# Optimization experiments

Measured on AMD Instinct MI355X. Metric: run time of the kernel, lower is better.

Reference implementation:

```python
import jax, jax.numpy as jnp
import numpy as np

NEG = -1e30  # log-space 'zero' that stays finite under autodiff
BLANK = 0


def _logsumexp3(a, b, c):
    m = jnp.maximum(jnp.maximum(a, b), c)
    return m + jnp.log(jnp.exp(a - m) + jnp.exp(b - m) + jnp.exp(c - m))


def setup_inputs() -> dict:
    key = jax.random.key(0)
    k1, k2, k3, k4 = jax.random.split(key, 4)
    T, B, C, S = 1024, 128, 96, 200
    logits = jax.random.normal(k1, (T, B, C), dtype=jnp.float32)
    log_probs = jax.nn.log_softmax(logits, axis=-1)  # CTC expects log-probs
    targets = jax.random.randint(k2, (B, S), 1, C, dtype=jnp.int32)  # labels in [1, C-1]
    input_lengths = jax.random.randint(k3, (B,), T // 2, T + 1, dtype=jnp.int32)
    target_lengths = jax.random.randint(k4, (B,), S // 2, S + 1, dtype=jnp.int32)
    return {"log_probs": log_probs, "targets": targets,
            "input_lengths": input_lengths, "target_lengths": target_lengths}


def ctc_loss(log_probs, targets, input_lengths, target_lengths):
    T, B, C = log_probs.shape
    S = targets.shape[1]
    L = 2 * S + 1  # extended target length (blanks interleaved)

    # Extended target sequence: blank, t0, blank, t1, ..., blank  -> [B, L]
    ext = jnp.zeros((B, L), dtype=targets.dtype).at[:, 1::2].set(targets)
    # Skip transition s-2 -> s allowed when ext[s] != blank and ext[s] != ext[s-2]
    ext_m2 = jnp.pad(ext[:, :-2], ((0, 0), (2, 0)), constant_values=BLANK)
    allow_skip = (ext != BLANK) & (ext != ext_m2) & (jnp.arange(L)[None, :] >= 2)

    emit0 = jnp.take_along_axis(log_probs[0], ext, axis=1)  # [B, L]
    alpha0 = jnp.full((B, L), NEG, dtype=log_probs.dtype)
    alpha0 = alpha0.at[:, 0].set(emit0[:, 0]).at[:, 1].set(emit0[:, 1])

    def step(alpha, lp_t):
        a1 = jnp.pad(alpha[:, :-1], ((0, 0), (1, 0)), constant_values=NEG)
        a2 = jnp.pad(alpha[:, :-2], ((0, 0), (2, 0)), constant_values=NEG)
        a2 = jnp.where(allow_skip, a2, NEG)
        emit = jnp.take_along_axis(lp_t, ext, axis=1)  # [B, L]
        new = _logsumexp3(alpha, a1, a2) + emit
        return new, new

    _, alphas_rest = jax.lax.scan(step, alpha0, log_probs[1:])  # [T-1, B, L]
    alphas = jnp.concatenate([alpha0[None], alphas_rest], axis=0)  # [T, B, L]

    # Gather alpha at t = input_length - 1 for each batch element -> [B, L]
    aT = alphas[input_lengths - 1, jnp.arange(B)]
    s_last = 2 * target_lengths  # index of trailing blank
    end_idx = jnp.stack([s_last - 1, s_last], axis=1)  # [B, 2]
    a_end = jnp.take_along_axis(aT, end_idx, axis=1)  # [B, 2]
    m = jnp.max(a_end, axis=1)
    ll = m + jnp.log(jnp.sum(jnp.exp(a_end - m[:, None]), axis=1))
    loss = -ll
    # zero_infinity=True: zero out non-finite (huge) losses
    loss = jnp.where(loss > 1e29, 0.0, loss)
    # reduction='mean': divide by target lengths, then mean over batch
    return jnp.mean(loss / target_lengths.astype(loss.dtype))


def reference(log_probs, targets, input_lengths, target_lengths):
    return ctc_loss(log_probs, targets, input_lengths, target_lengths)
```

## Files before the change

### kernel.cpp

```cpp
#include <hip/hip_runtime.h>
#include <hip/hip_fp16.h>

#define NEGV  (-1e30f)
#define LOG2E 1.44269504088896340736f
#define LN2F  0.69314718055994530942f

constexpr int Tn = 1024;
constexpr int Bn = 128;
constexpr int Cn = 96;
constexpr int Sn = 200;
constexpr int Ln = 2 * Sn + 1;
constexpr int W  = 7;
constexpr int CH = 16;
constexpr int NCH = Tn / CH;

__device__ __forceinline__ float fexp2(float x) {
#if __has_builtin(__builtin_amdgcn_exp2f)
    return __builtin_amdgcn_exp2f(x);
#else
    return exp2f(x);
#endif
}
__device__ __forceinline__ float flog2(float x) {
#if __has_builtin(__builtin_amdgcn_logf)
    return __builtin_amdgcn_logf(x);
#else
    return __log2f(x);
#endif
}
__device__ __forceinline__ float2 cvt2(unsigned u) {
    const __half2 h = *reinterpret_cast<const __half2*>(&u);
    return __half22float2(h);
}

__device__ __forceinline__ float shup1(float x) {
    return __int_as_float(__builtin_amdgcn_update_dpp(
        0, __float_as_int(x), 0x138, 0xf, 0xf, false));
}

__device__ __forceinline__ float wave_max_dpp_to_lane63(float x) {
    #define DPP_MAX(ctrl)                                                   \
        x = fmaxf(x, __int_as_float(__builtin_amdgcn_update_dpp(            \
                __float_as_int(x), __float_as_int(x), (ctrl), 0xf, 0xf, false)))
    DPP_MAX(0x111);
    DPP_MAX(0x112);
    DPP_MAX(0x114);
    DPP_MAX(0x118);
    DPP_MAX(0x142);
    DPP_MAX(0x143);
    #undef DPP_MAX
    return x;
}

__global__ __launch_bounds__(256, 1) void ctc_fused_kernel(
    const float* __restrict__ lp,
    const int*   __restrict__ tg,
    const int*   __restrict__ il,
    const int*   __restrict__ tl,
    float*       __restrict__ out_pb)
{
    const int b    = blockIdx.x;
    const int w    = threadIdx.x >> 6;
    const int lane = threadIdx.x & 63;

    __shared__ __half buf[2][CH][512];
    __shared__ float  endv[2];

    float a0v = 0.f, a1v = 0.f, a2v = 0.f, a3v = 0.f, a4v = 0.f, a5v = 0.f, a6v = 0.f;
    float pm1 = 0.f, pm2 = 0.f;
    float g0 = 0.f, g1 = 0.f, g2 = 0.f, g3 = 0.f, g4 = 0.f, g5 = 0.f, g6 = 0.f;
    float zl = 0.f, g1z = 0.f, g0z = 0.f;
    int   K = 0, k_cap = 0, t = 1;
    int   inlen = 1 << 30, tlen = 1, ee0 = -1, ee1 = -1;

    int   cidx[W] = {0, 0, 0, 0, 0, 0, 0};
    bool  liv[W]  = {false, false, false, false, false, false, false};
    float rE[6][W];
    int   pw = 0;

#define P_LOAD(CHK)                                                          \
    {                                                                        \
        _Pragma("unroll")                                                    \
        for (int k = 0; k < 6; ++k) {                                        \
            const int r_ = pw + 3 * k;                                       \
            const int t_ = (r_ < CH) ? ((CHK) * CH + r_) : (Tn - 1);         \
            const float* src_ = lp + ((size_t)t_ * Bn + b) * Cn;             \
            _Pragma("unroll")                                                \
            for (int j = 0; j < W; ++j) rE[k][j] = src_[cidx[j]];            \
        }                                                                    \
    }

#define P_GATH(CHK)                                                          \
    {                                                                        \
        const int bb_ = (CHK) & 1;                                           \
        _Pragma("unroll")                                                    \
        for (int k = 0; k < 6; ++k) {                                        \
            const int r_ = pw + 3 * k;                                       \
            if (r_ < CH) {                                                   \
                unsigned us_[8];                                             \
                _Pragma("unroll")                                            \
                for (int j = 0; j < W; ++j) {                                \
                    const float pr_ = liv[j] ? fexp2(rE[k][j] * LOG2E) : 0.0f; \
                    us_[j] = __half_as_ushort(__float2half(pr_));            \
                }                                                            \
                us_[7] = 0;                                                  \
                uint4 v_;                                                    \
                v_.x = us_[0] | (us_[1] << 16);                              \
                v_.y = us_[2] | (us_[3] << 16);                              \
                v_.z = us_[4] | (us_[5] << 16);                              \
                v_.w = us_[6] | (us_[7] << 16);                              \
                *reinterpret_cast<uint4*>(&buf[bb_][r_][lane * 8]) = v_;     \
            }                                                                \
        }                                                                    \
    }

    if (w == 0) {
        if (lane == 0) { endv[0] = 0.0f; endv[1] = 0.0f; }
        inlen = il[b];
        tlen  = tl[b];
        ee0 = 2 * tlen - 1;
        ee1 = 2 * tlen;
        auto mk_gate = [&](int j) -> float {
            const int s = lane * W + j;
            if (s < Ln && (s & 1) && s >= 3) {
                const int kk = s >> 1;
                if (tg[b * Sn + kk] != tg[b * Sn + kk - 1]) return 1.0f;
            }
            return 0.0f;
        };
        g0 = mk_gate(0); g1 = mk_gate(1); g2 = mk_gate(2); g3 = mk_gate(3);
        g4 = mk_gate(4); g5 = mk_gate(5); g6 = mk_gate(6);
        zl  = (lane == 0) ? 0.0f : 1.0f;
        g1z = g1 * zl;
        g0z = g0 * zl;
    } else {
        pw = w - 1;
        #pragma unroll
        for (int j = 0; j < W; ++j) {
            const int s = lane * W + j;
            cidx[j] = (s < Ln && (s & 1)) ? tg[b * Sn + (s >> 1)] : 0;
            liv[j]  = (s < Ln);
        }
        P_LOAD(0);
        P_GATH(0);
        P_LOAD(1);
    }
    __syncthreads();

#define CAP(J, AJ) { const int s_ = lane * W + (J);                          \
                     if (s_ == ee0) endv[0] = (AJ);                          \
                     if (s_ == ee1) endv[1] = (AJ); }

#define CSTEP(V)                                                             \
  {                                                                          \
    float2 f_;                                                               \
    f_ = cvt2((V).x); const float e0m = f_.x, e1m = f_.y;                    \
    f_ = cvt2((V).y); const float e2m = f_.x, e3m = f_.y;                    \
    f_ = cvt2((V).z); const float e4m = f_.x, e5m = f_.y;                    \
    f_ = cvt2((V).w); const float e6m = f_.x;                                \
    const float n6 = fmaf(g6, a4v, a6v + a5v) * e6m;                         \
    const float n5 = fmaf(g5, a3v, a5v + a4v) * e5m;                         \
    const float npm1 = shup1(n6);               \
    const float npm2 = shup1(n5);                                            \
    const float n4 = fmaf(g4, a2v, a4v + a3v) * e4m;                         \
    const float n3 = fmaf(g3, a1v, a3v + a2v) * e3m;                         \
    const float n2 = fmaf(g2, a0v, a2v + a1v) * e2m;                         \
    const float n1 = fmaf(g1z, pm1, a1v + a0v) * e1m;                        \
    const float n0 = fmaf(g0z, pm2, fmaf(zl, pm1, a0v)) * e0m;               \
    a6v = n6; a5v = n5; a4v = n4; a3v = n3; a2v = n2; a1v = n1; a0v = n0;    \
    pm1 = npm1; pm2 = npm2;                                                  \
    if (t == inlen - 1) {                                                    \
      CAP(0, a0v); CAP(1, a1v); CAP(2, a2v); CAP(3, a3v);                    \
      CAP(4, a4v); CAP(5, a5v); CAP(6, a6v);                                 \
      k_cap = K;                                                             \
    }                                                                        \
    ++t;                                                                     \
  }

#define BMAX(J, AJ) { const int s_ = lane * W + (J);                         \
                      if (s_ >= ell && s_ <= ee1) mx = fmaxf(mx, (AJ)); }

#define RESCALE()                                                            \
  {                                                                          \
    const int ell = (2 * tlen - 1) - 2 * (inlen - t);                        \
    float mx = 0.0f;                                                         \
    BMAX(0, a0v); BMAX(1, a1v); BMAX(2, a2v); BMAX(3, a3v);                  \
    BMAX(4, a4v); BMAX(5, a5v); BMAX(6, a6v);                                \
    const float mxr = wave_max_dpp_to_lane63(mx);                            \
    const int  smx = __builtin_amdgcn_readlane(__float_as_int(mxr), 63);     \
    const int  eb  = (smx >> 23) & 0xff;                                     \
    const bool nz  = (smx > 0) && (eb < 255);                                \
    const float scale = nz ? __int_as_float((254 - eb) << 23) : 1.0f;        \
    K += nz ? (127 - eb) : 0;                                                \
    a0v *= scale; a1v *= scale; a2v *= scale; a3v *= scale;                  \
    a4v *= scale; a5v *= scale; a6v *= scale;                                \
    pm1 *= scale; pm2 *= scale;                                              \
  }

    for (int c = 0; c < NCH; ++c) {
        if (w == 0) {
            const uint4* rp =
                reinterpret_cast<const uint4*>(&buf[c & 1][0][0]) + lane;
            uint4 q[8];
            if (c == 0) {
                a0v = (lane == 0) ? __half2float(buf[0][0][0]) : 0.0f;
                a1v = (lane == 0) ? __half2float(buf[0][0][1]) : 0.0f;
                #pragma unroll
                for (int k = 0; k < 8; ++k) q[k] = rp[(k + 1) * 64];
                #pragma unroll
                for (int i = 1; i < CH; ++i) {
                    const uint4 v = q[(i - 1) & 7];
                    if (i < 8) q[(i - 1) & 7] = rp[(i + 8) * 64];
                    CSTEP(v);
                    if (i == 7 || i == 15) RESCALE();
                }
            } else {
                #pragma unroll
                for (int k = 0; k < 8; ++k) q[k] = rp[k * 64];
                #pragma unroll
                for (int i = 0; i < CH; ++i) {
                    const uint4 v = q[i & 7];
                    if (i < 8) q[i & 7] = rp[(i + 8) * 64];
                    CSTEP(v);
                    if (i == 7 || i == 15) RESCALE();
                }
            }
        } else {
            if (c + 1 < NCH) {
                P_GATH(c + 1);
                if (c + 2 < NCH) P_LOAD(c + 2);
            }
        }
        __syncthreads();
    }

#undef RESCALE
#undef BMAX
#undef CSTEP
#undef CAP
#undef P_GATH
#undef P_LOAD

    if (w == 0 && lane == 0) {
        const float sum = endv[0] + endv[1];
        const float ll2 = flog2(sum) - (float)k_cap;
        float lb = -(ll2 * LN2F);
        if (lb > 1e29f || !(lb == lb)) lb = 0.0f;
        out_pb[b] = lb / (float)tlen;
    }
}

__global__ __launch_bounds__(448) void ctc_fallback_kernel(
    const float* __restrict__ lp, const int* __restrict__ tg,
    const int* __restrict__ il, const int* __restrict__ tl,
    float* __restrict__ out_pb)
{
    const int b   = blockIdx.x;
    const int tid = threadIdx.x;

    __shared__ float alpha[2][Ln];
    __shared__ float lprow[2][Cn];
    __shared__ float endv[2];

    const int inlen = il[b];
    const int tlen  = tl[b];
    const int e0 = 2 * tlen - 1;
    const int e1 = 2 * tlen;

    const bool active = (tid < Ln);
    int  myclass = 0;
    bool allow   = false;
    if (active && (tid & 1)) {
        const int k = tid >> 1;
        myclass = tg[b * Sn + k];
        if (tid >= 3) allow = (myclass != tg[b * Sn + k - 1]);
    }

    const float* lpb = lp + (size_t)b * Cn;
    if (tid < Cn) lprow[0][tid] = lpb[tid];

    float vv[4] = {0.f, 0.f, 0.f, 0.f};
    if (tid < Cn) {
        vv[1] = lpb[(size_t)1 * Bn * Cn + tid];
        vv[2] = lpb[(size_t)2 * Bn * Cn + tid];
        vv[3] = lpb[(size_t)3 * Bn * Cn + tid];
        vv[0] = lpb[(size_t)4 * Bn * Cn + tid];
    }
    __syncthreads();
    if (active) alpha[0][tid] = (tid < 2) ? lprow[0][myclass] : NEGV;

    int cur = 0;
    #pragma unroll 4
    for (int t = 1; t < Tn; ++t) {
        if (tid < Cn) {
            lprow[t & 1][tid] = vv[t & 3];
            if (t + 4 < Tn)
                vv[t & 3] = lpb[(size_t)(t + 4) * Bn * Cn + tid];
        }
        __syncthreads();
        if (active) {
            const float a0 = alpha[cur][tid];
            const float a1 = (tid >= 1) ? alpha[cur][tid - 1] : NEGV;
            const float a2 = allow ? alpha[cur][tid - 2] : NEGV;
            const float m  = fmaxf(a0, fmaxf(a1, a2));
            const float nv = m + __logf(__expf(a0 - m) + __expf(a1 - m) + __expf(a2 - m))
                           + lprow[t & 1][myclass];
            alpha[cur ^ 1][tid] = nv;
            if (t == inlen - 1) {
                if (tid == e0) endv[0] = nv;
                if (tid == e1) endv[1] = nv;
            }
        }
        cur ^= 1;
    }
    __syncthreads();

    if (tid == 0) {
        const float x = endv[0], y = endv[1];
        const float m = fmaxf(x, y);
        const float ll = m + __logf(__expf(x - m) + __expf(y - m));
        float lb = -ll;
        if (lb > 1e29f) lb = 0.f;
        out_pb[b] = lb / (float)tlen;
    }
}

__global__ void reduce_mean_kernel(const float* __restrict__ pb,
                                   float* __restrict__ out)
{
    const int l = threadIdx.x;
    float s = pb[l] + pb[l + 64];
    #pragma unroll
    for (int o = 32; o; o >>= 1) s += __shfl_down(s, o);
    if (l == 0) out[0] = s * (1.0f / (float)Bn);
}

extern "C" void kernel_launch(void* const* d_in, const int* in_sizes, int n_in,
                              void* d_out, int out_size, void* d_ws, size_t ws_size,
                              hipStream_t stream)
{
    const float* lp = (const float*)d_in[0];
    const int*   tg = (const int*)d_in[1];
    const int*   il = (const int*)d_in[2];
    const int*   tl = (const int*)d_in[3];
    float* out = (float*)d_out;

    if (ws_size >= 4096) {
        float* pb = (float*)d_ws;
        ctc_fused_kernel<<<Bn, 256, 0, stream>>>(lp, tg, il, tl, pb);
        reduce_mean_kernel<<<1, 64, 0, stream>>>(pb, out);
    } else {
        float* pb = (float*)d_ws;
        ctc_fallback_kernel<<<Bn, 448, 0, stream>>>(lp, tg, il, tl, pb);
        reduce_mean_kernel<<<1, 64, 0, stream>>>(pb, out);
    }
}
```

Before: 201.6 us.

## Double-buffer producer registers and use a lighter LDS-only barrier

Producer waves now hold two register sets, so the global loads for chunk c+2 are issued before the exp/convert/store of chunk c+1 instead of after it. This hides global load latency across a whole chunk rather than only behind the gather. The chunk loop is unrolled by two so the LDS buffer index and register set are compile-time constants. The __syncthreads is replaced by a custom barrier that waits only on lgkmcnt, letting outstanding global loads stay in flight across the barrier. The cost is extra register pressure in the producer waves.

```diff
diff --git a/kernel.cpp b/kernel.cpp
--- a/kernel.cpp
+++ b/kernel.cpp
@@ -52,6 +52,14 @@
     return x;
 }
 
+#define PCBAR()                                                              \
+    do {                                                                     \
+        __builtin_amdgcn_sched_barrier(0);                                   \
+        asm volatile("s_waitcnt lgkmcnt(0)" ::: "memory");                   \
+        __builtin_amdgcn_s_barrier();                                        \
+        __builtin_amdgcn_sched_barrier(0);                                   \
+    } while (0)
+
 __global__ __launch_bounds__(256, 1) void ctc_fused_kernel(
     const float* __restrict__ lp,
     const int*   __restrict__ tg,
@@ -75,10 +83,10 @@
 
     int   cidx[W] = {0, 0, 0, 0, 0, 0, 0};
     bool  liv[W]  = {false, false, false, false, false, false, false};
-    float rE[6][W];
+    float rEA[6][W], rEB[6][W];
     int   pw = 0;
 
-#define P_LOAD(CHK)                                                          \
+#define P_LOAD_SET(CHK, RS)                                                  \
     {                                                                        \
         _Pragma("unroll")                                                    \
         for (int k = 0; k < 6; ++k) {                                        \
@@ -86,11 +94,11 @@
             const int t_ = (r_ < CH) ? ((CHK) * CH + r_) : (Tn - 1);         \
             const float* src_ = lp + ((size_t)t_ * Bn + b) * Cn;             \
             _Pragma("unroll")                                                \
-            for (int j = 0; j < W; ++j) rE[k][j] = src_[cidx[j]];            \
+            for (int j = 0; j < W; ++j) RS[k][j] = src_[cidx[j]];            \
         }                                                                    \
     }
 
-#define P_GATH(CHK)                                                          \
+#define P_GATH_SET(CHK, RS)                                                  \
     {                                                                        \
         const int bb_ = (CHK) & 1;                                           \
         _Pragma("unroll")                                                    \
@@ -100,7 +108,7 @@
                 unsigned us_[8];                                             \
                 _Pragma("unroll")                                            \
                 for (int j = 0; j < W; ++j) {                                \
-                    const float pr_ = liv[j] ? fexp2(rE[k][j] * LOG2E) : 0.0f; \
+                    const float pr_ = liv[j] ? fexp2(RS[k][j] * LOG2E) : 0.0f; \
                     us_[j] = __half_as_ushort(__float2half(pr_));            \
                 }                                                            \
                 us_[7] = 0;                                                  \
@@ -141,11 +149,11 @@
             cidx[j] = (s < Ln && (s & 1)) ? tg[b * Sn + (s >> 1)] : 0;
             liv[j]  = (s < Ln);
         }
-        P_LOAD(0);
-        P_GATH(0);
-        P_LOAD(1);
-    }
-    __syncthreads();
+        P_LOAD_SET(0, rEA);
+        P_GATH_SET(0, rEA);
+        P_LOAD_SET(1, rEB);
+    }
+    PCBAR();
 
 #define CAP(J, AJ) { const int s_ = lane * W + (J);                          \
                      if (s_ == ee0) endv[0] = (AJ);                          \
@@ -197,49 +205,64 @@
     pm1 *= scale; pm2 *= scale;                                              \
   }
 
-    for (int c = 0; c < NCH; ++c) {
+#define CONSUME(BB)                                                          \
+  {                                                                          \
+    const uint4* rp = reinterpret_cast<const uint4*>(&buf[BB][0][0]) + lane; \
+    uint4 q[8];                                                              \
+    _Pragma("unroll")                                                        \
+    for (int k = 0; k < 8; ++k) q[k] = rp[k * 64];                           \
+    _Pragma("unroll")                                                        \
+    for (int i = 0; i < CH; ++i) {                                           \
+        const uint4 v = q[i & 7];                                            \
+        if (i < 8) q[i & 7] = rp[(i + 8) * 64];                              \
+        CSTEP(v);                                                            \
+        if (i == 7 || i == 15) RESCALE();                                    \
+    }                                                                        \
+  }
+
+#define CONSUME0()                                                           \
+  {                                                                          \
+    const uint4* rp = reinterpret_cast<const uint4*>(&buf[0][0][0]) + lane;  \
+    a0v = (lane == 0) ? __half2float(buf[0][0][0]) : 0.0f;                   \
+    a1v = (lane == 0) ? __half2float(buf[0][0][1]) : 0.0f;                   \
+    uint4 q[8];                                                              \
+    _Pragma("unroll")                                                        \
+    for (int k = 0; k < 8; ++k) q[k] = rp[(k + 1) * 64];                     \
+    _Pragma("unroll")                                                        \
+    for (int i = 1; i < CH; ++i) {                                           \
+        const uint4 v = q[(i - 1) & 7];                                      \
+        if (i < 8) q[(i - 1) & 7] = rp[(i + 8) * 64];                        \
+        CSTEP(v);                                                            \
+        if (i == 7 || i == 15) RESCALE();                                    \
+    }                                                                        \
+  }
+
+    for (int c = 0; c < NCH; c += 2) {
         if (w == 0) {
-            const uint4* rp =
-                reinterpret_cast<const uint4*>(&buf[c & 1][0][0]) + lane;
-            uint4 q[8];
-            if (c == 0) {
-                a0v = (lane == 0) ? __half2float(buf[0][0][0]) : 0.0f;
-                a1v = (lane == 0) ? __half2float(buf[0][0][1]) : 0.0f;
-                #pragma unroll
-                for (int k = 0; k < 8; ++k) q[k] = rp[(k + 1) * 64];
-                #pragma unroll
-                for (int i = 1; i < CH; ++i) {
-                    const uint4 v = q[(i - 1) & 7];
-                    if (i < 8) q[(i - 1) & 7] = rp[(i + 8) * 64];
-                    CSTEP(v);
-                    if (i == 7 || i == 15) RESCALE();
-                }
-            } else {
-                #pragma unroll
-                for (int k = 0; k < 8; ++k) q[k] = rp[k * 64];
-                #pragma unroll
-                for (int i = 0; i < CH; ++i) {
-                    const uint4 v = q[i & 7];
-                    if (i < 8) q[i & 7] = rp[(i + 8) * 64];
-                    CSTEP(v);
-                    if (i == 7 || i == 15) RESCALE();
-                }
-            }
+            if (c == 0) { CONSUME0(); }
+            else        { CONSUME(0); }
         } else {
-            if (c + 1 < NCH) {
-                P_GATH(c + 1);
-                if (c + 2 < NCH) P_LOAD(c + 2);
-            }
-        }
-        __syncthreads();
-    }
-
+            if (c + 2 < NCH) P_LOAD_SET(c + 2, rEA);
+            P_GATH_SET(c + 1, rEB);
+        }
+        PCBAR();
+        if (w == 0) {
+            CONSUME(1);
+        } else {
+            if (c + 3 < NCH) P_LOAD_SET(c + 3, rEB);
+            if (c + 2 < NCH) P_GATH_SET(c + 2, rEA);
+        }
+        PCBAR();
+    }
+
+#undef CONSUME0
+#undef CONSUME
 #undef RESCALE
 #undef BMAX
 #undef CSTEP
 #undef CAP
-#undef P_GATH
-#undef P_LOAD
+#undef P_GATH_SET
+#undef P_LOAD_SET
 
     if (w == 0 && lane == 0) {
         const float sum = endv[0] + endv[1];
```

Result: slower. 209.6 us (+4.0%).
